# Kernel tuning notes

Measured on AMD Instinct MI355X. Metric: run time of the kernel, lower is better.

The kernel has to match this reference:

```python
import jax, jax.numpy as jnp
import numpy as np

B_J0 = 0.01
BETA = 1.8   # isAdapt=1
LENS = 0.5
DT = 1.0
IN_SIZE = 1
STRIDE = IN_SIZE
T = 784 // STRIDE
HID = (512, 512, 512)
OUT = 10
N = 256


def _create_general_mask(dim, c_min, c_max, min_dc, max_dc, phase_max, T):
    # faithful port of ASRNN_general.create_general_mask (numpy, static)
    dcs = np.linspace(min_dc, max_dc, dim)
    cycles = np.linspace(c_min, c_max, dim)
    shifts = np.linspace(0.0, float(int(phase_max * c_max)), dim)
    rows = []
    for cyc, dc, ps in zip(cycles, dcs, shifts):
        cyc = int(np.round(cyc))
        on = int(np.round(dc * cyc))
        pat = [1.0] * on + [0.0] * (cyc - on)
        ps = int(np.round(ps))
        if ps > 0:
            pat = pat[-ps:] + pat[:-ps]
        rows.append(pat * (T // cyc) + pat[: T % cyc])
    return np.asarray(rows, dtype=np.float32)  # [dim, T]

MASK1 = jnp.asarray(_create_general_mask(HID[0], 2, 8, 0.2, 0.8, 0.5, T))
MASK2 = jnp.asarray(_create_general_mask(HID[1], 4, 16, 0.2, 0.8, 0.5, T))
MASK3 = jnp.asarray(_create_general_mask(HID[2], 8, 32, 0.2, 0.8, 0.5, T))

# per-step input gather indices (faithful to the start_idx branch in forward)
_starts = np.arange(T) * STRIDE
_IDX = np.where(_starts[:, None] < T - IN_SIZE,
                _starts[:, None] + np.arange(IN_SIZE)[None, :],
                (784 - IN_SIZE) + np.arange(IN_SIZE)[None, :])  # [T, IN]


@jax.custom_vjp
def act_fun(x):
    return (x > 0.0).astype(x.dtype)

def _act_fwd(x):
    return (x > 0.0).astype(x.dtype), x

def _act_bwd(x, g):
    return (g * (jnp.abs(x) < LENS).astype(g.dtype),)

act_fun.defvjp(_act_fwd, _act_bwd)


def _mem_update(inputs, mem, spike, tau_adp, b, tau_m, mask_t):
    alpha = jnp.exp(-DT / tau_m)
    ro = jnp.exp(-DT / tau_adp)
    b_new = ro * b + (1.0 - ro) * spike
    Bth = B_J0 + BETA * b_new
    mem_new = mem * alpha + (1.0 - alpha) * inputs - Bth * spike * DT
    mem_new = jnp.where(mask_t == 0.0, mem, mem_new)
    spike_new = act_fun(mem_new - Bth) * mask_t
    return mem_new, spike_new, b_new


def _forward(x, wi1, bi1, wh1, bh1, wi2, bi2, wh2, bh2, wi3, bi3, wo, bo,
             tau_adp1, tau_adp2, tau_adp3, tau_m1, tau_m2, tau_m3):
    n = x.shape[0]
    x_seq = jnp.transpose(x[:, _IDX], (1, 0, 2))            # [T, N, IN]
    pre1 = jnp.einsum('tni,hi->tnh', x_seq, wi1) + bi1       # [T, N, H1]

    def step_fn(carry, xs):
        mem1, spk1, b1, mem2, spk2, b2, mem3, spk3, b3, out_sum, s1, s2, s3 = carry
        p1, m1, m2, m3 = xs
        h1_in = p1 + spk1 @ wh1.T + bh1
        mem1, spk1, b1 = _mem_update(h1_in, mem1, spk1, tau_adp1, b1, tau_m1, m1)
        h2_in = spk1 @ wi2.T + bi2 + spk2 @ wh2.T + bh2
        mem2, spk2, b2 = _mem_update(h2_in, mem2, spk2, tau_adp2, b2, tau_m2, m2)
        h3_in = spk2 @ wi3.T + bi3
        mem3, spk3, b3 = _mem_update(h3_in, mem3, spk3, tau_adp3, b3, tau_m3, m3)
        out_sum = out_sum + spk3 @ wo.T + bo
        return (mem1, spk1, b1, mem2, spk2, b2, mem3, spk3, b3,
                out_sum, s1 + spk1, s2 + spk2, s3 + spk3), None

    z = lambda h: jnp.zeros((n, h), x.dtype)
    f = lambda h: jnp.full((n, h), B_J0, x.dtype)
    carry0 = (z(HID[0]), z(HID[0]), f(HID[0]),
              z(HID[1]), z(HID[1]), f(HID[1]),
              z(HID[2]), z(HID[2]), f(HID[2]),
              jnp.zeros((n, OUT), x.dtype), z(HID[0]), z(HID[1]), z(HID[2]))
    xs = (pre1, MASK1.T, MASK2.T, MASK3.T)
    carry, _ = jax.lax.scan(step_fn, carry0, xs)
    out_sum, s1, s2, s3 = carry[9], carry[10], carry[11], carry[12]
    outputs = out_sum / T
    layer_fr = jnp.stack([s1.sum() / (n * HID[0] * T),
                          s2.sum() / (n * HID[1] * T),
                          s3.sum() / (n * HID[2] * T)])
    return outputs, s1 / T, s2 / T, s3 / T, layer_fr


def setup_inputs() -> dict:
    key = jax.random.key(0)
    ks = jax.random.split(key, 20)
    def xav(k, shp):
        fan_in, fan_out = shp[1], shp[0]
        s = np.sqrt(2.0 / (fan_in + fan_out))
        return jax.random.normal(k, shp, jnp.float32) * s
    return {
        'x': jax.random.uniform(ks[0], (N, 784), jnp.float32),
        'wi1': xav(ks[1], (HID[0], IN_SIZE)), 'bi1': jnp.zeros((HID[0],), jnp.float32),
        'wh1': xav(ks[2], (HID[0], HID[0])), 'bh1': jnp.zeros((HID[0],), jnp.float32),
        'wi2': xav(ks[3], (HID[1], HID[0])), 'bi2': jnp.zeros((HID[1],), jnp.float32),
        'wh2': xav(ks[4], (HID[1], HID[1])), 'bh2': jnp.zeros((HID[1],), jnp.float32),
        'wi3': xav(ks[5], (HID[2], HID[1])), 'bi3': jnp.zeros((HID[2],), jnp.float32),
        'wo': xav(ks[6], (OUT, HID[2])), 'bo': jnp.zeros((OUT,), jnp.float32),
        'tau_adp1': 700.0 + 25.0 * jax.random.normal(ks[7], (HID[0],), jnp.float32),
        'tau_adp2': 700.0 + 25.0 * jax.random.normal(ks[8], (HID[1],), jnp.float32),
        'tau_adp3': 700.0 + 25.0 * jax.random.normal(ks[9], (HID[2],), jnp.float32),
        'tau_m1': 5.0 + jax.random.normal(ks[10], (HID[0],), jnp.float32),
        'tau_m2': 5.0 + jax.random.normal(ks[11], (HID[1],), jnp.float32),
        'tau_m3': 5.0 + jax.random.normal(ks[12], (HID[2],), jnp.float32),
    }


def reference(x, wi1, bi1, wh1, bh1, wi2, bi2, wh2, bh2, wi3, bi3, wo, bo,
              tau_adp1, tau_adp2, tau_adp3, tau_m1, tau_m2, tau_m3):
    return _forward(x, wi1, bi1, wh1, bh1, wi2, bi2, wh2, bh2, wi3, bi3, wo, bo,
                    tau_adp1, tau_adp2, tau_adp3, tau_m1, tau_m2, tau_m3)
```

## Files before the change

kernel.cpp:

```cpp
#include <hip/hip_runtime.h>
#include <stdint.h>

#pragma clang fp contract(off)


static constexpr int    TS      = 784;
static constexpr size_t WS_WT1  = 0;
static constexpr size_t WS_WT2A = 1u << 20;
static constexpr size_t WS_WT2B = 2u << 20;
static constexpr size_t WS_WT3  = 3u << 20;
static constexpr size_t WS_M1   = 4u << 20;
static constexpr size_t WS_M2   = WS_M1 + (size_t)TS * 512;
static constexpr size_t WS_M3   = WS_M2 + (size_t)TS * 512;
static constexpr size_t WS_FRP  = WS_M3 + (size_t)TS * 512;

__device__ __forceinline__ float exp_np(float x) {
  float q = rintf(x * 1.442695040f);
  float r = __fmaf_rn(-q, 0.693359375f, x);
  r = __fmaf_rn(-q, -2.12194440e-4f, r);
  float r2 = r * r;
  float p = 1.9875691500e-4f;
  p = __fmaf_rn(p, r, 1.3981999507e-3f);
  p = __fmaf_rn(p, r, 8.3334519073e-3f);
  p = __fmaf_rn(p, r, 4.1665795894e-2f);
  p = __fmaf_rn(p, r, 1.6666665459e-1f);
  p = __fmaf_rn(p, r, 5.0000001201e-1f);
  p = __fmaf_rn(p, r2, r);
  p = p + 1.0f;
  return ldexpf(p, (int)q);
}

__device__ __forceinline__ int mask_val(int l, int h, int t) {
  const double cmin = (l == 0) ? 2.0 : ((l == 1) ? 4.0 : 8.0);
  const double cmax = (l == 0) ? 8.0 : ((l == 1) ? 16.0 : 32.0);
  const double smax = (l == 0) ? 4.0 : ((l == 1) ? 8.0 : 16.0);
  const double cD = (cmax - cmin) / 511.0;
  const double dD = (0.8 - 0.2) / 511.0;
  const double sD = smax / 511.0;
  const double hd = (double)h;
  double cycd = (h == 511) ? cmax : __dadd_rn(cmin, __dmul_rn(hd, cD));
  double dcd  = (h == 511) ? 0.8  : __dadd_rn(0.2,  __dmul_rn(hd, dD));
  double psd  = (h == 511) ? smax : __dmul_rn(hd, sD);
  int cyc = __double2int_rn(cycd);
  int on  = __double2int_rn(__dmul_rn(dcd, (double)cyc));
  int ps  = __double2int_rn(psd);
  int eff = (ps >= cyc) ? 0 : ps;
  int pos = (t % cyc) - eff;
  if (pos < 0) pos += cyc;
  return (pos < on) ? 1 : 0;
}

__global__ void setup_masks(char* __restrict__ ws) {
  const int t = blockIdx.x, tid = threadIdx.x;
  uint8_t* m1 = (uint8_t*)(ws + WS_M1);
  uint8_t* m2 = (uint8_t*)(ws + WS_M2);
  uint8_t* m3 = (uint8_t*)(ws + WS_M3);
  for (int h = tid; h < 512; h += 256) {
    m1[t * 512 + h] = (uint8_t)mask_val(0, h, t);
    m2[t * 512 + h] = (uint8_t)mask_val(1, h, t);
    m3[t * 512 + h] = (uint8_t)mask_val(2, h, t);
  }
}

__global__ void transpose_kernel(const float* __restrict__ wh1,
                                 const float* __restrict__ wi2,
                                 const float* __restrict__ wh2,
                                 const float* __restrict__ wi3,
                                 char* __restrict__ ws) {
  const int k = blockIdx.x;
  const int m = blockIdx.y;
  const float* W = (m == 0) ? wh1 : (m == 1) ? wi2 : (m == 2) ? wh2 : wi3;
  float* T = (float*)(ws + (size_t)m * (1u << 20));
  for (int j = threadIdx.x; j < 512; j += 256)
    T[(size_t)k * 512 + j] = W[(size_t)j * 512 + k];
}

__device__ __forceinline__ uint32_t upd32(float hin, uint32_t mk, uint32_t osp,
                                          float al, float om, float r, float omr,
                                          float& memv, float& bv) {
  float t1 = r * bv;
  float bn = osp ? (t1 + omr) : t1;
  float bt = 1.8f * bn;
  float Bth = 0.01f + bt;
  float m1 = memv * al;
  float m2 = om * hin;
  float m3 = m1 + m2;
  float mn = osp ? (m3 - Bth) : m3;
  if (!mk) mn = memv;
  uint32_t sn = (mk && (mn - Bth) > 0.0f) ? 1u : 0u;
  memv = mn; bv = bn;
  return sn;
}

__device__ __forceinline__ float gather(const float* __restrict__ wT, int h,
                                        const ushort* kl, int cnt) {
  const float* base = wT + h;
  float s = 0.0f;
  int i = 0;
  for (; i + 16 <= cnt; i += 16) {
    float w0  = base[(size_t)kl[i + 0]  << 9];
    float w1  = base[(size_t)kl[i + 1]  << 9];
    float w2  = base[(size_t)kl[i + 2]  << 9];
    float w3  = base[(size_t)kl[i + 3]  << 9];
    float w4  = base[(size_t)kl[i + 4]  << 9];
    float w5  = base[(size_t)kl[i + 5]  << 9];
    float w6  = base[(size_t)kl[i + 6]  << 9];
    float w7  = base[(size_t)kl[i + 7]  << 9];
    float w8  = base[(size_t)kl[i + 8]  << 9];
    float w9  = base[(size_t)kl[i + 9]  << 9];
    float w10 = base[(size_t)kl[i + 10] << 9];
    float w11 = base[(size_t)kl[i + 11] << 9];
    float w12 = base[(size_t)kl[i + 12] << 9];
    float w13 = base[(size_t)kl[i + 13] << 9];
    float w14 = base[(size_t)kl[i + 14] << 9];
    float w15 = base[(size_t)kl[i + 15] << 9];
    s = s + w0;  s = s + w1;  s = s + w2;  s = s + w3;
    s = s + w4;  s = s + w5;  s = s + w6;  s = s + w7;
    s = s + w8;  s = s + w9;  s = s + w10; s = s + w11;
    s = s + w12; s = s + w13; s = s + w14; s = s + w15;
  }
  for (; i + 4 <= cnt; i += 4) {
    float w0 = base[(size_t)kl[i + 0] << 9];
    float w1 = base[(size_t)kl[i + 1] << 9];
    float w2 = base[(size_t)kl[i + 2] << 9];
    float w3 = base[(size_t)kl[i + 3] << 9];
    s = s + w0; s = s + w1; s = s + w2; s = s + w3;
  }
  for (; i < cnt; ++i) s = s + base[(size_t)kl[i] << 9];
  return s;
}

__global__ __launch_bounds__(512, 1) void rnn_block(
    const float* __restrict__ x,
    const float* __restrict__ wi1, const float* __restrict__ bi1,
    const float* __restrict__ bh1,
    const float* __restrict__ bi2, const float* __restrict__ bh2,
    const float* __restrict__ bi3,
    const float* __restrict__ wo, const float* __restrict__ bo,
    const float* __restrict__ ta1, const float* __restrict__ ta2,
    const float* __restrict__ ta3, const float* __restrict__ tm1,
    const float* __restrict__ tm2, const float* __restrict__ tm3,
    char* __restrict__ ws, float* __restrict__ d_out) {
  const int n = blockIdx.x;
  const int h = threadIdx.x;
  const float* WT1  = (const float*)(ws + WS_WT1);
  const float* WT2A = (const float*)(ws + WS_WT2A);
  const float* WT2B = (const float*)(ws + WS_WT2B);
  const float* WT3  = (const float*)(ws + WS_WT3);
  const uint8_t* M1 = (const uint8_t*)(ws + WS_M1);
  const uint8_t* M2 = (const uint8_t*)(ws + WS_M2);
  const uint8_t* M3 = (const uint8_t*)(ws + WS_M3);

  __shared__ uint64_t bm1s[8], bm2s[8], bm3s[8];
  __shared__ ushort kl1s[512], kl2s[512];
  __shared__ int cnt1s, cnt2s;
  __shared__ float woS[10 * 513];
  __shared__ double red[512];

  for (int i = h; i < 5120; i += 512) woS[(i / 512) * 513 + (i % 512)] = wo[i];
  if (h == 0) { cnt1s = 0; cnt2s = 0; }

  float al1 = exp_np(-1.0f / tm1[h]), om1 = 1.0f - al1;
  float ro1 = exp_np(-1.0f / ta1[h]), omr1 = 1.0f - ro1;
  float al2 = exp_np(-1.0f / tm2[h]), om2 = 1.0f - al2;
  float ro2 = exp_np(-1.0f / ta2[h]), omr2 = 1.0f - ro2;
  float al3 = exp_np(-1.0f / tm3[h]), om3 = 1.0f - al3;
  float ro3 = exp_np(-1.0f / ta3[h]), omr3 = 1.0f - ro3;
  float wi1v = wi1[h], bi1v = bi1[h], bh1v = bh1[h];
  float bi2v = bi2[h], bh2v = bh2[h], bi3v = bi3[h];
  float bo_v = (h < 80 && (h & 7) == 0) ? bo[h >> 3] : 0.0f;

  float mem1 = 0.0f, b1 = 0.01f, c1 = 0.0f;
  float mem2 = 0.0f, b2 = 0.01f, c2 = 0.0f;
  float mem3 = 0.0f, b3 = 0.01f, c3 = 0.0f;
  uint32_t sp1 = 0, sp2 = 0, sp3 = 0;
  float outv = 0.0f;

  const float* xrow = x + (size_t)n * 784;
  __syncthreads();

  for (int t = 0; t < TS; ++t) {
    const uint32_t mk1 = M1[t * 512 + h];
    const uint32_t mk2 = M2[t * 512 + h];
    const uint32_t mk3 = M3[t * 512 + h];
    const float xv = xrow[t];

    float acc1 = 0.0f;
    if (mk1 && cnt1s > 0) acc1 = gather(WT1, h, kl1s, cnt1s);
    float p1 = xv * wi1v;
    p1 = p1 + bi1v;
    p1 = p1 + acc1;
    p1 = p1 + bh1v;
    uint32_t sn1 = upd32(p1, mk1, sp1, al1, om1, ro1, omr1, mem1, b1);
    sp1 = sn1; c1 += (float)sn1;
    uint64_t bal1 = __ballot(sn1);
    if ((h & 63) == 0) bm1s[h >> 6] = bal1;
    __syncthreads();
    if (h < 8) {
      int off = 0;
      for (int w2 = 0; w2 < h; ++w2) off += __builtin_popcountll(bm1s[w2]);
      uint64_t v = bm1s[h];
      int base = h * 64;
      while (v) { int b = __builtin_ctzll(v); v &= v - 1; kl1s[off++] = (ushort)(base + b); }
      if (h == 7) cnt1s = off;
    }
    __syncthreads();

    float a1 = 0.0f, a2 = 0.0f;
    if (mk2) {
      if (cnt1s > 0) a1 = gather(WT2A, h, kl1s, cnt1s);
      if (cnt2s > 0) a2 = gather(WT2B, h, kl2s, cnt2s);
    }
    float p2 = a1 + bi2v;
    p2 = p2 + a2;
    p2 = p2 + bh2v;
    uint32_t sn2 = upd32(p2, mk2, sp2, al2, om2, ro2, omr2, mem2, b2);
    sp2 = sn2; c2 += (float)sn2;
    uint64_t bal2 = __ballot(sn2);
    if ((h & 63) == 0) bm2s[h >> 6] = bal2;
    __syncthreads();
    if (h < 8) {
      int off = 0;
      for (int w2 = 0; w2 < h; ++w2) off += __builtin_popcountll(bm2s[w2]);
      uint64_t v = bm2s[h];
      int base = h * 64;
      while (v) { int b = __builtin_ctzll(v); v &= v - 1; kl2s[off++] = (ushort)(base + b); }
      if (h == 7) cnt2s = off;
    }
    __syncthreads();

    float a3 = 0.0f;
    if (mk3 && cnt2s > 0) a3 = gather(WT3, h, kl2s, cnt2s);
    float p3 = a3 + bi3v;
    uint32_t sn3 = upd32(p3, mk3, sp3, al3, om3, ro3, omr3, mem3, b3);
    sp3 = sn3; c3 += (float)sn3;
    uint64_t bal3 = __ballot(sn3);
    if ((h & 63) == 0) bm3s[h >> 6] = bal3;
    __syncthreads();

    if (h < 80) {
      const int w = h & 7;
      uint64_t v = bm3s[w];
      float s = 0.0f;
      const float* wrow = &woS[(h >> 3) * 513 + w * 64];
      while (v) { int b = __builtin_ctzll(v); v &= v - 1; s = s + wrow[b]; }
      s += __shfl_down(s, 4, 8);
      s += __shfl_down(s, 2, 8);
      s += __shfl_down(s, 1, 8);
      if (w == 0) { float vv = outv + s; outv = vv + bo_v; }
    }
  }

  d_out[2560 + (size_t)n * 512 + h]          = c1 / 784.0f;
  d_out[2560 + 131072 + (size_t)n * 512 + h] = c2 / 784.0f;
  d_out[2560 + 262144 + (size_t)n * 512 + h] = c3 / 784.0f;
  if (h < 80 && (h & 7) == 0) d_out[(size_t)n * 10 + (h >> 3)] = outv / 784.0f;

  double* FRP = (double*)(ws + WS_FRP);
  red[h] = (double)c1;
  __syncthreads();
  for (int wd = 256; wd > 0; wd >>= 1) {
    if (h < wd) red[h] += red[h + wd];
    __syncthreads();
  }
  if (h == 0) FRP[n * 3 + 0] = red[0];
  __syncthreads();
  red[h] = (double)c2;
  __syncthreads();
  for (int wd = 256; wd > 0; wd >>= 1) {
    if (h < wd) red[h] += red[h + wd];
    __syncthreads();
  }
  if (h == 0) FRP[n * 3 + 1] = red[0];
  __syncthreads();
  red[h] = (double)c3;
  __syncthreads();
  for (int wd = 256; wd > 0; wd >>= 1) {
    if (h < wd) red[h] += red[h + wd];
    __syncthreads();
  }
  if (h == 0) FRP[n * 3 + 2] = red[0];
}

__global__ void finalize_fr(char* __restrict__ ws, float* __restrict__ d_out) {
  const int l = threadIdx.x;
  if (l >= 3) return;
  const double* FRP = (const double*)(ws + WS_FRP);
  double s = 0.0;
  for (int n = 0; n < 256; ++n) s += FRP[n * 3 + l];
  d_out[395776 + l] = (float)(s / (131072.0 * 784.0));
}

extern "C" void kernel_launch(void* const* d_in, const int* in_sizes, int n_in,
                              void* d_out, int out_size, void* d_ws, size_t ws_size,
                              hipStream_t stream) {
  (void)in_sizes; (void)n_in; (void)out_size; (void)ws_size;
  const float* x   = (const float*)d_in[0];
  const float* wi1 = (const float*)d_in[1];
  const float* bi1 = (const float*)d_in[2];
  const float* wh1 = (const float*)d_in[3];
  const float* bh1 = (const float*)d_in[4];
  const float* wi2 = (const float*)d_in[5];
  const float* bi2 = (const float*)d_in[6];
  const float* wh2 = (const float*)d_in[7];
  const float* bh2 = (const float*)d_in[8];
  const float* wi3 = (const float*)d_in[9];
  const float* bi3 = (const float*)d_in[10];
  const float* wo  = (const float*)d_in[11];
  const float* bo  = (const float*)d_in[12];
  const float* ta1 = (const float*)d_in[13];
  const float* ta2 = (const float*)d_in[14];
  const float* ta3 = (const float*)d_in[15];
  const float* tm1 = (const float*)d_in[16];
  const float* tm2 = (const float*)d_in[17];
  const float* tm3 = (const float*)d_in[18];
  char*  ws  = (char*)d_ws;
  float* out = (float*)d_out;

  hipLaunchKernelGGL(setup_masks, dim3(TS), dim3(256), 0, stream, ws);
  hipLaunchKernelGGL(transpose_kernel, dim3(512, 4), dim3(256), 0, stream,
                     wh1, wi2, wh2, wi3, ws);
  hipLaunchKernelGGL(rnn_block, dim3(256), dim3(512), 0, stream,
                     x, wi1, bi1, bh1, bi2, bh2, bi3, wo, bo,
                     ta1, ta2, ta3, tm1, tm2, tm3, ws, out);
  hipLaunchKernelGGL(finalize_fr, dim3(1), dim3(64), 0, stream, ws, out);
}
```

Before: 4.970 ms.

## Build spike index lists in parallel and interleave layer-2 dual gathers

Spike-list compaction moves from a serial loop over 8 threads to every thread computing its own rank with popcounts and scattering its index. Each thread also keeps the spike counts in registers, which removes the shared count variables. The layer-2 gathers from the two weight matrices are interleaved eight at a time to raise memory-level parallelism. The summation order within each accumulator is unchanged, so results stay bitwise identical, at the cost of some extra per-thread popcount work.

Result: faster. 4.178 ms (median of 2 runs) (-15.9%).

```diff
diff --git a/kernel.cpp b/kernel.cpp
--- a/kernel.cpp
+++ b/kernel.cpp
@@ -92,11 +92,27 @@
   return sn;
 }
 
-__device__ __forceinline__ float gather(const float* __restrict__ wT, int h,
-                                        const ushort* kl, int cnt) {
-  const float* base = wT + h;
-  float s = 0.0f;
-  int i = 0;
+__device__ __forceinline__ int expand_list(const uint64_t* __restrict__ bm,
+                                           uint32_t mysp, int h,
+                                           ushort* __restrict__ kl) {
+  const int wh = h >> 6, bpos = h & 63;
+  int cnt = 0, rank = 0;
+#pragma unroll
+  for (int w = 0; w < 8; ++w) {
+    uint64_t v = bm[w];
+    int pc = __builtin_popcountll(v);
+    if (w < wh) rank += pc;
+    cnt += pc;
+  }
+  rank += __builtin_popcountll(bm[wh] & ((1ull << bpos) - 1ull));
+  if (mysp) kl[rank] = (ushort)h;
+  return cnt;
+}
+
+__device__ __forceinline__ float gather_from(const float* __restrict__ base,
+                                             const ushort* kl, int from, int cnt,
+                                             float s) {
+  int i = from;
   for (; i + 16 <= cnt; i += 16) {
     float w0  = base[(size_t)kl[i + 0]  << 9];
     float w1  = base[(size_t)kl[i + 1]  << 9];
@@ -153,12 +169,10 @@
 
   __shared__ uint64_t bm1s[8], bm2s[8], bm3s[8];
   __shared__ ushort kl1s[512], kl2s[512];
-  __shared__ int cnt1s, cnt2s;
   __shared__ float woS[10 * 513];
   __shared__ double red[512];
 
   for (int i = h; i < 5120; i += 512) woS[(i / 512) * 513 + (i % 512)] = wo[i];
-  if (h == 0) { cnt1s = 0; cnt2s = 0; }
 
   float al1 = exp_np(-1.0f / tm1[h]), om1 = 1.0f - al1;
   float ro1 = exp_np(-1.0f / ta1[h]), omr1 = 1.0f - ro1;
@@ -174,6 +188,7 @@
   float mem2 = 0.0f, b2 = 0.01f, c2 = 0.0f;
   float mem3 = 0.0f, b3 = 0.01f, c3 = 0.0f;
   uint32_t sp1 = 0, sp2 = 0, sp3 = 0;
+  int cnt1 = 0, cnt2 = 0;
   float outv = 0.0f;
 
   const float* xrow = x + (size_t)n * 784;
@@ -186,7 +201,7 @@
     const float xv = xrow[t];
 
     float acc1 = 0.0f;
-    if (mk1 && cnt1s > 0) acc1 = gather(WT1, h, kl1s, cnt1s);
+    if (mk1 && cnt1 > 0) acc1 = gather_from(WT1 + h, kl1s, 0, cnt1, 0.0f);
     float p1 = xv * wi1v;
     p1 = p1 + bi1v;
     p1 = p1 + acc1;
@@ -196,20 +211,39 @@
     uint64_t bal1 = __ballot(sn1);
     if ((h & 63) == 0) bm1s[h >> 6] = bal1;
     __syncthreads();
-    if (h < 8) {
-      int off = 0;
-      for (int w2 = 0; w2 < h; ++w2) off += __builtin_popcountll(bm1s[w2]);
-      uint64_t v = bm1s[h];
-      int base = h * 64;
-      while (v) { int b = __builtin_ctzll(v); v &= v - 1; kl1s[off++] = (ushort)(base + b); }
-      if (h == 7) cnt1s = off;
-    }
+    cnt1 = expand_list(bm1s, sn1, h, kl1s);
     __syncthreads();
 
     float a1 = 0.0f, a2 = 0.0f;
     if (mk2) {
-      if (cnt1s > 0) a1 = gather(WT2A, h, kl1s, cnt1s);
-      if (cnt2s > 0) a2 = gather(WT2B, h, kl2s, cnt2s);
+      const float* bA = WT2A + h;
+      const float* bB = WT2B + h;
+      int iA = 0, iB = 0;
+      while (iA + 8 <= cnt1 && iB + 8 <= cnt2) {
+        float wa0 = bA[(size_t)kl1s[iA + 0] << 9];
+        float wa1 = bA[(size_t)kl1s[iA + 1] << 9];
+        float wa2 = bA[(size_t)kl1s[iA + 2] << 9];
+        float wa3 = bA[(size_t)kl1s[iA + 3] << 9];
+        float wa4 = bA[(size_t)kl1s[iA + 4] << 9];
+        float wa5 = bA[(size_t)kl1s[iA + 5] << 9];
+        float wa6 = bA[(size_t)kl1s[iA + 6] << 9];
+        float wa7 = bA[(size_t)kl1s[iA + 7] << 9];
+        float wb0 = bB[(size_t)kl2s[iB + 0] << 9];
+        float wb1 = bB[(size_t)kl2s[iB + 1] << 9];
+        float wb2 = bB[(size_t)kl2s[iB + 2] << 9];
+        float wb3 = bB[(size_t)kl2s[iB + 3] << 9];
+        float wb4 = bB[(size_t)kl2s[iB + 4] << 9];
+        float wb5 = bB[(size_t)kl2s[iB + 5] << 9];
+        float wb6 = bB[(size_t)kl2s[iB + 6] << 9];
+        float wb7 = bB[(size_t)kl2s[iB + 7] << 9];
+        a1 = a1 + wa0; a1 = a1 + wa1; a1 = a1 + wa2; a1 = a1 + wa3;
+        a1 = a1 + wa4; a1 = a1 + wa5; a1 = a1 + wa6; a1 = a1 + wa7;
+        a2 = a2 + wb0; a2 = a2 + wb1; a2 = a2 + wb2; a2 = a2 + wb3;
+        a2 = a2 + wb4; a2 = a2 + wb5; a2 = a2 + wb6; a2 = a2 + wb7;
+        iA += 8; iB += 8;
+      }
+      a1 = gather_from(bA, kl1s, iA, cnt1, a1);
+      a2 = gather_from(bB, kl2s, iB, cnt2, a2);
     }
     float p2 = a1 + bi2v;
     p2 = p2 + a2;
@@ -219,18 +253,11 @@
     uint64_t bal2 = __ballot(sn2);
     if ((h & 63) == 0) bm2s[h >> 6] = bal2;
     __syncthreads();
-    if (h < 8) {
-      int off = 0;
-      for (int w2 = 0; w2 < h; ++w2) off += __builtin_popcountll(bm2s[w2]);
-      uint64_t v = bm2s[h];
-      int base = h * 64;
-      while (v) { int b = __builtin_ctzll(v); v &= v - 1; kl2s[off++] = (ushort)(base + b); }
-      if (h == 7) cnt2s = off;
-    }
+    cnt2 = expand_list(bm2s, sn2, h, kl2s);
     __syncthreads();
 
     float a3 = 0.0f;
-    if (mk3 && cnt2s > 0) a3 = gather(WT3, h, kl2s, cnt2s);
+    if (mk3 && cnt2 > 0) a3 = gather_from(WT3 + h, kl2s, 0, cnt2, 0.0f);
     float p3 = a3 + bi3v;
     uint32_t sn3 = upd32(p3, mk3, sp3, al3, om3, ro3, omr3, mem3, b3);
     sp3 = sn3; c3 += (float)sn3;
```
